# Kernel tuning notes

Measured on AMD Instinct MI355X. Metric: run time of the kernel, lower is better.

The kernel has to match this reference:

```python
import jax, jax.numpy as jnp
import numpy as np

HID = 256   # hidden_dim
P = 16      # pool_size
EPS = 1e-5


def _ln(x, g, b):
    m = x.mean(-1, keepdims=True)
    v = x.var(-1, keepdims=True)
    return (x - m) * jax.lax.rsqrt(v + EPS) * g + b


def setup_inputs() -> dict:
    key = jax.random.key(0)
    ks = jax.random.split(key, 12)
    B, Cf, H, W = 8, 512, 64, 64
    Cg = Cf // 2
    Co = Cf // 2
    s = 0.02
    d = {}
    d['e_f'] = jax.random.normal(ks[0], (B, Cf, H, W), jnp.float32)
    d['e_g'] = jax.random.normal(ks[1], (B, Cg, H, W), jnp.float32)
    d['l_feat'] = jax.random.normal(ks[2], (B, 768, 20), jnp.float32)
    d['l_mask'] = jnp.ones((B, 20, 1), jnp.float32)
    d['ln_f_g'] = jnp.ones((Cf,), jnp.float32)
    d['ln_f_b'] = jnp.zeros((Cf,), jnp.float32)
    d['ln_g_g'] = jnp.ones((Cg,), jnp.float32)
    d['ln_g_b'] = jnp.zeros((Cg,), jnp.float32)
    d['wq'] = jax.random.normal(ks[3], (Cf, HID), jnp.float32) * s
    d['bq'] = jnp.zeros((HID,), jnp.float32)
    d['wk'] = jax.random.normal(ks[4], (Cg, HID), jnp.float32) * s
    d['bk'] = jnp.zeros((HID,), jnp.float32)
    d['wv'] = jax.random.normal(ks[5], (Cg, HID), jnp.float32) * s
    d['bv'] = jnp.zeros((HID,), jnp.float32)
    d['wo'] = jax.random.normal(ks[6], (HID, HID), jnp.float32) * s
    d['bo'] = jnp.zeros((HID,), jnp.float32)
    d['dw_k'] = jax.random.normal(ks[7], (HID, 1, 3, 3), jnp.float32) * s  # depthwise kernel (OIHW, I=1)
    d['efp_w'] = jax.random.normal(ks[8], (HID, Cf), jnp.float32) * s     # 1x1 conv v_channels->hidden
    d['efp_b'] = jnp.zeros((HID,), jnp.float32)
    d['outc_w'] = jax.random.normal(ks[9], (Co, HID), jnp.float32) * s    # 1x1 conv hidden->out
    d['outc_b'] = jnp.zeros((Co,), jnp.float32)
    d['bn_g'] = jnp.ones((Co,), jnp.float32)
    d['bn_b'] = jnp.zeros((Co,), jnp.float32)
    d['bn_m'] = jnp.zeros((Co,), jnp.float32)
    d['bn_v'] = jnp.ones((Co,), jnp.float32)
    return d


def reference(e_f, e_g, l_feat, l_mask, ln_f_g, ln_f_b, ln_g_g, ln_g_b,
              wq, bq, wk, bk, wv, bv, wo, bo, dw_k, efp_w, efp_b,
              outc_w, outc_b, bn_g, bn_b, bn_m, bn_v):
    B, Cf, H, W = e_f.shape
    # Q = w_qi(LN(e_f))                                  (B, HW, HID)
    q = _ln(e_f.transpose(0, 2, 3, 1), ln_f_g, ln_f_b).reshape(B, H * W, Cf) @ wq + bq
    # K/V projections from LN(e_g)
    g = _ln(e_g.transpose(0, 2, 3, 1), ln_g_g, ln_g_b).reshape(B, H * W, -1)
    k = (g @ wk + bk).reshape(B, H, W, HID)
    v = (g @ wv + bv).reshape(B, H, W, HID)
    # 16x16 max/avg pooling -> (B, Hp*Wp, HID)
    k = jnp.max(k.reshape(B, H // P, P, W // P, P, HID), axis=(2, 4)).reshape(B, -1, HID)
    v = jnp.mean(v.reshape(B, H // P, P, W // P, P, HID), axis=(2, 4)).reshape(B, -1, HID)
    # pooled attention
    attn = jax.nn.softmax(jnp.einsum('bqd,bkd->bqk', q, k) * (HID ** -0.5), axis=-1)
    a_i = jnp.einsum('bqk,bkd->bqd', attn, v)  # (B, HW, HID)
    # depthwise 3x3 conv on Q (NCHW)
    q_nchw = q.reshape(B, H, W, HID).transpose(0, 3, 1, 2)
    dw = jax.lax.conv_general_dilated(q_nchw, dw_k, (1, 1), [(1, 1), (1, 1)],
                                      feature_group_count=HID)
    combined = dw + a_i.reshape(B, H, W, HID).transpose(0, 3, 1, 2)
    comb = combined.transpose(0, 2, 3, 1).reshape(B, H * W, HID) @ wo + bo
    comb = comb.reshape(B, H, W, HID).transpose(0, 3, 1, 2)
    # 1x1 proj of e_f, elementwise gate
    efp = jnp.einsum('bchw,oc->bohw', e_f, efp_w) + efp_b[None, :, None, None]
    e_a = efp * comb
    # out: 1x1 conv + BN (inference) + ReLU (dropout inactive in eval)
    out = jnp.einsum('bchw,oc->bohw', e_a, outc_w) + outc_b[None, :, None, None]
    scale = (bn_g * jax.lax.rsqrt(bn_v + EPS))[None, :, None, None]
    out = (out - bn_m[None, :, None, None]) * scale + bn_b[None, :, None, None]
    return jax.nn.relu(out)
```

## Files before the change

kernel.cpp:

```cpp
#include <hip/hip_runtime.h>
#include <math.h>

#define EPS 1e-5f

typedef __attribute__((ext_vector_type(8))) short bf16x8;
typedef __attribute__((ext_vector_type(4))) float f32x4;

__device__ __forceinline__ unsigned short f2bf(float f) {
    unsigned int u = __float_as_uint(f);
    u += 0x7fff + ((u >> 16) & 1);
    return (unsigned short)(u >> 16);
}
__device__ __forceinline__ float bf2f(unsigned short h) {
    return __uint_as_float(((unsigned int)h) << 16);
}
__device__ __forceinline__ float lof(unsigned int u) {
    return __uint_as_float(u << 16);
}
__device__ __forceinline__ float hif(unsigned int u) {
    return __uint_as_float(u & 0xffff0000u);
}
__device__ __forceinline__ void async16(void* lds, const void* g) {
    __builtin_amdgcn_global_load_lds(
        (const __attribute__((address_space(1))) unsigned int*)g,
        (__attribute__((address_space(3))) unsigned int*)lds, 16, 0, 0);
}

__global__ __launch_bounds__(256) void prep_all(
    const float* __restrict__ lnfg, const float* __restrict__ lnfb,
    const float* __restrict__ wq, const float* __restrict__ bq,
    const float* __restrict__ efpw, const float* __restrict__ efpb,
    const float* __restrict__ lngg, const float* __restrict__ lngb,
    const float* __restrict__ wk, const float* __restrict__ bk,
    const float* __restrict__ wv, const float* __restrict__ bv,
    const float* __restrict__ wo, const float* __restrict__ outcw,
    const float* __restrict__ outcb, const float* __restrict__ bng,
    const float* __restrict__ bnb, const float* __restrict__ bnm,
    const float* __restrict__ bnv, const float* __restrict__ dwk,
    unsigned short* __restrict__ Wb1t, unsigned short* __restrict__ Wb2t,
    unsigned short* __restrict__ Wot, unsigned short* __restrict__ Woc,
    float* __restrict__ dwt,
    float* __restrict__ cs1, float* __restrict__ cst1,
    float* __restrict__ cs2, float* __restrict__ cst2,
    float* __restrict__ scv, float* __restrict__ shv)
{
    int idx = blockIdx.x * 256 + threadIdx.x;
    if (idx < 262144) {
        int n = idx >> 9, k = idx & 511;
        float v = (n < 256) ? lnfg[k] * wq[k * 256 + n]
                            : efpw[(size_t)(n - 256) * 512 + k];
        Wb1t[idx] = f2bf(v);
    } else if (idx < 327680) {
        int j = idx - 262144; int n = j >> 8, k = j & 255;
        Wb2t[j] = f2bf(lngg[k] * wk[k * 256 + n]);
    } else if (idx < 393216) {
        int j = idx - 327680; int n = j >> 8, k = j & 255;
        Wot[j] = f2bf(wo[k * 256 + n]);
    } else if (idx < 458752) {
        int j = idx - 393216;
        Woc[j] = f2bf(outcw[j]);
    } else if (idx < 461056) {
        int j = idx - 458752; int tap = j >> 8, ch = j & 255;
        dwt[j] = dwk[ch * 9 + tap];
    } else if (idx < 462336) {
        int j = idx - 461056;
        if (j < 256) {
            int n = j; float cs = 0.f, ct = 0.f;
            for (int k = 0; k < 512; k++) {
                float w = wq[k * 256 + n];
                cs += lnfg[k] * w; ct += lnfb[k] * w;
            }
            cs1[n] = cs; cst1[n] = ct + bq[n];
        } else if (j < 512) {
            cs1[j] = 0.f; cst1[j] = efpb[j - 256];
        } else if (j < 768) {
            int n = j - 512; float cs = 0.f, ct = 0.f;
            for (int k = 0; k < 256; k++) {
                float w = wk[k * 256 + n];
                cs += lngg[k] * w; ct += lngb[k] * w;
            }
            cs2[n] = cs; cst2[n] = ct + bk[n];
        } else if (j < 1024) {
            int n = j - 768; float cs = 0.f, ct = 0.f;
            for (int k = 0; k < 256; k++) {
                float w = wv[k * 256 + n];
                cs += lngg[k] * w; ct += lngb[k] * w;
            }
            cs2[256 + n] = cs; cst2[256 + n] = ct + bv[n];
        } else {
            int n = j - 1024;
            float s = bng[n] * rsqrtf(bnv[n] + EPS);
            scv[n] = s;
            shv[n] = (outcb[n] - bnm[n]) * s + bnb[n];
        }
    }
}

__global__ __launch_bounds__(256) void transpose_fg(
    const float* __restrict__ ef, const float* __restrict__ eg,
    unsigned short* __restrict__ ef_bf, unsigned short* __restrict__ eg_bf,
    float* __restrict__ pf, float* __restrict__ pfq,
    float* __restrict__ pg, float* __restrict__ pgq)
{
    __shared__ float tile[16384];
    int id = blockIdx.x;
    const float* src; unsigned short* dst; float* ps; float* pq;
    int C, cblk, b, p0;
    if (id < 1024) {
        src = ef; dst = ef_bf; ps = pf; pq = pfq; C = 512;
        b = id >> 7; cblk = (id >> 4) & 7; p0 = (id & 15) * 256;
    } else {
        id -= 1024;
        src = eg; dst = eg_bf; ps = pg; pq = pgq; C = 256;
        b = id >> 6; cblk = (id >> 4) & 3; p0 = (id & 15) * 256;
    }
    int c0 = cblk * 64;
    const float* s = src + ((size_t)b * C + c0) * 4096 + p0;
    int t = threadIdx.x;
    int wave = t >> 6, lane = t & 63;

    float4 rr[16];
#pragma unroll
    for (int i = 0; i < 16; i++) {
        int c = wave * 16 + i;
        rr[i] = *(const float4*)(s + (size_t)c * 4096 + lane * 4);
    }
#pragma unroll
    for (int i = 0; i < 16; i++) {
        int c = wave * 16 + i;
        int rq = (c + (c >> 3)) & 63;
        *(float4*)&tile[c * 256 + (((lane + rq) & 63) << 2)] = rr[i];
    }
    __syncthreads();

    {
        int pq4 = t >> 2, pr4 = t & 3;
        float sm = 0.f, sq = 0.f;
#pragma unroll
        for (int c = 0; c < 64; c++) {
            int rq = (c + (c >> 3)) & 63;
            float v = tile[c * 256 + (((pq4 + rq) & 63) << 2) + pr4];
            sm += v; sq += v * v;
        }
        ps[cblk * 32768 + b * 4096 + p0 + t] = sm;
        pq[cblk * 32768 + b * 4096 + p0 + t] = sq;
    }

    unsigned short* d = dst + ((size_t)(b * 4096 + p0)) * C + c0;
    int pr = t >> 3, c8 = (t & 7) * 8;
#pragma unroll
    for (int i = 0; i < 8; i++) {
        int p = i * 32 + pr;
        int pq4 = p >> 2, pr4 = p & 3;
        float v[8];
#pragma unroll
        for (int j = 0; j < 8; j++) {
            int c = c8 + j;
            int rq = (c + (c >> 3)) & 63;
            v[j] = tile[c * 256 + (((pq4 + rq) & 63) << 2) + pr4];
        }
        uint4 pk;
        pk.x = (unsigned)f2bf(v[0]) | ((unsigned)f2bf(v[1]) << 16);
        pk.y = (unsigned)f2bf(v[2]) | ((unsigned)f2bf(v[3]) << 16);
        pk.z = (unsigned)f2bf(v[4]) | ((unsigned)f2bf(v[5]) << 16);
        pk.w = (unsigned)f2bf(v[6]) | ((unsigned)f2bf(v[7]) << 16);
        *(uint4*)(d + (size_t)p * C + c8) = pk;
    }
}

template<int K>
__device__ __forceinline__ void mfma_core(
    const unsigned short* __restrict__ A, const unsigned short* __restrict__ Bt,
    int m0, int n0, unsigned short* As, unsigned short* Bs, f32x4 acc[4][4])
{
    const int tid = threadIdx.x;
    const int wave = tid >> 6, lane = tid & 63;
    const int wm = (wave & 1) * 64, wn = (wave >> 1) * 64;
#pragma unroll
    for (int i = 0; i < 4; i++)
#pragma unroll
        for (int j = 0; j < 4; j++) acc[i][j] = (f32x4){0.f, 0.f, 0.f, 0.f};

    const int srow = wave * 32 + (lane >> 3);
    const int sg = (lane & 7) ^ ((lane >> 3) & 7);
    const unsigned short* ga = A + (size_t)(m0 + srow) * K + sg * 8;
    const unsigned short* gb = Bt + (size_t)(n0 + srow) * K + sg * 8;

    for (int k0 = 0; k0 < K; k0 += 64) {
#pragma unroll
        for (int t = 0; t < 4; t++) {
            async16(As + (wave * 32 + t * 8) * 64, ga + (size_t)t * 8 * K + k0);
            async16(Bs + (wave * 32 + t * 8) * 64, gb + (size_t)t * 8 * K + k0);
        }
        __syncthreads();
#pragma unroll
        for (int ks = 0; ks < 2; ks++) {
            bf16x8 af[4], bfr[4];
            int kb = ks * 4 + (lane >> 4);
            int slot = (kb ^ (lane & 7)) * 8;
#pragma unroll
            for (int i = 0; i < 4; i++) {
                int m = wm + i * 16 + (lane & 15);
                af[i] = *(const bf16x8*)&As[m * 64 + slot];
                int n = wn + i * 16 + (lane & 15);
                bfr[i] = *(const bf16x8*)&Bs[n * 64 + slot];
            }
#pragma unroll
            for (int i = 0; i < 4; i++)
#pragma unroll
                for (int j = 0; j < 4; j++)
                    acc[i][j] = __builtin_amdgcn_mfma_f32_16x16x32_bf16(
                        af[i], bfr[j], acc[i][j], 0, 0, 0);
        }
        __syncthreads();
    }
}

__global__ __launch_bounds__(256, 2) void gemm1_mfma(
    const unsigned short* __restrict__ ef_bf, const unsigned short* __restrict__ Wb1t,
    const float* __restrict__ cs1, const float* __restrict__ cst1,
    const float* __restrict__ pf, const float* __restrict__ pfq,
    unsigned short* __restrict__ qbuf, unsigned short* __restrict__ efpbuf)
{
    __shared__ unsigned short As[128 * 64];
    __shared__ unsigned short Bs[256 * 64];
    __shared__ float smf[128], srf[128];
    f32x4 acc[4][8];
    const int tid = threadIdx.x;
    const int wave = tid >> 6, lane = tid & 63;
    const int wm = (wave & 1) * 64, wn = (wave >> 1) * 128;
    const int m0 = blockIdx.x * 128, n0 = blockIdx.y * 256;

    if (tid < 128) {
        int gm = m0 + tid;
        float s = 0.f, q = 0.f;
#pragma unroll
        for (int i = 0; i < 8; i++) { s += pf[i * 32768 + gm]; q += pfq[i * 32768 + gm]; }
        float m = s * (1.f / 512.f);
        smf[tid] = m;
        srf[tid] = rsqrtf(q * (1.f / 512.f) - m * m + EPS);
    }

#pragma unroll
    for (int i = 0; i < 4; i++)
#pragma unroll
        for (int j = 0; j < 8; j++) acc[i][j] = (f32x4){0.f, 0.f, 0.f, 0.f};

    const int srow = lane >> 3;
    const int sg = (lane & 7) ^ (srow & 7);
    const unsigned short* ga = ef_bf + (size_t)(m0 + wave * 32 + srow) * 512 + sg * 8;
    const unsigned short* gb = Wb1t + (size_t)(n0 + wave * 64 + srow) * 512 + sg * 8;

    for (int k0 = 0; k0 < 512; k0 += 64) {
#pragma unroll
        for (int t = 0; t < 4; t++)
            async16(As + (wave * 32 + t * 8) * 64, ga + (size_t)t * 8 * 512 + k0);
#pragma unroll
        for (int t = 0; t < 8; t++)
            async16(Bs + (wave * 64 + t * 8) * 64, gb + (size_t)t * 8 * 512 + k0);
        __syncthreads();
#pragma unroll
        for (int ks = 0; ks < 2; ks++) {
            bf16x8 af[4], bfr[8];
            int kb = ks * 4 + (lane >> 4);
            int slot = (kb ^ (lane & 7)) * 8;
#pragma unroll
            for (int i = 0; i < 4; i++)
                af[i] = *(const bf16x8*)&As[(wm + i * 16 + (lane & 15)) * 64 + slot];
#pragma unroll
            for (int j = 0; j < 8; j++)
                bfr[j] = *(const bf16x8*)&Bs[(wn + j * 16 + (lane & 15)) * 64 + slot];
#pragma unroll
            for (int i = 0; i < 4; i++)
#pragma unroll
                for (int j = 0; j < 8; j++)
                    acc[i][j] = __builtin_amdgcn_mfma_f32_16x16x32_bf16(
                        af[i], bfr[j], acc[i][j], 0, 0, 0);
        }
        __syncthreads();
    }

    bool isq = (n0 == 0);
#pragma unroll
    for (int i = 0; i < 4; i++) {
#pragma unroll
        for (int r = 0; r < 4; r++) {
            int lm = wm + i * 16 + ((lane >> 4) * 4) + r;
            int gm = m0 + lm;
            float mean = smf[lm], rs = srf[lm];
#pragma unroll
            for (int j = 0; j < 8; j++) {
                int nn = wn + j * 16 + (lane & 15);
                float v = acc[i][j][r];
                if (isq) {
                    int n = nn;
                    float o = rs * (v - mean * cs1[n]) + cst1[n];
                    qbuf[(size_t)gm * 256 + nn] = f2bf(o);
                } else {
                    int n = nn + 256;
                    efpbuf[(size_t)gm * 256 + nn] = f2bf(v + cst1[n]);
                }
            }
        }
    }
}

__global__ __launch_bounds__(256) void gemm2k_mfma(
    const unsigned short* __restrict__ eg_bf, const unsigned short* __restrict__ Wb2t,
    const float* __restrict__ cs2, const float* __restrict__ cst2,
    const float* __restrict__ pg, const float* __restrict__ pgq,
    float* __restrict__ mg, float* __restrict__ rg,
    unsigned short* __restrict__ kfull)
{
    __shared__ unsigned short As[8192], Bs[8192];
    __shared__ float smg[128], srg[128];
    f32x4 acc[4][4];
    int m0 = blockIdx.x * 128, n0 = blockIdx.y * 128;
    int tid = threadIdx.x;

    if (tid < 128) {
        int gm = m0 + tid;
        float s = 0.f, q = 0.f;
#pragma unroll
        for (int i = 0; i < 4; i++) { s += pg[i * 32768 + gm]; q += pgq[i * 32768 + gm]; }
        float m = s * (1.f / 256.f);
        float r = rsqrtf(q * (1.f / 256.f) - m * m + EPS);
        smg[tid] = m; srg[tid] = r;
        if (n0 == 0) { mg[gm] = m; rg[gm] = r; }
    }

    mfma_core<256>(eg_bf, Wb2t, m0, n0, As, Bs, acc);
    int lane = tid & 63, wave = tid >> 6;
    int wm = (wave & 1) * 64, wn = (wave >> 1) * 64;
#pragma unroll
    for (int i = 0; i < 4; i++) {
#pragma unroll
        for (int r = 0; r < 4; r++) {
            int lm = wm + i * 16 + ((lane >> 4) * 4) + r;
            int gm = m0 + lm;
            float mean = smg[lm], rs = srg[lm];
#pragma unroll
            for (int j = 0; j < 4; j++) {
                int n = n0 + wn + j * 16 + (lane & 15);
                float o = rs * (acc[i][j][r] - mean * cs2[n]) + cst2[n];
                kfull[(size_t)gm * 256 + n] = f2bf(o);
            }
        }
    }
}

__global__ __launch_bounds__(256) void gemm34_mfma(
    const unsigned short* __restrict__ comb, const unsigned short* __restrict__ Wot,
    const float* __restrict__ bo, const unsigned short* __restrict__ efp,
    const unsigned short* __restrict__ Woc,
    const float* __restrict__ scv, const float* __restrict__ shv,
    float* __restrict__ outp)
{
    __shared__ unsigned short As[64 * 64];
    __shared__ unsigned short Bs[256 * 64];
    __shared__ unsigned short eat[64 * 256];
    const int tid = threadIdx.x;
    const int wave = tid >> 6, lane = tid & 63;
    const int m0 = blockIdx.x * 64;

    const int srow = lane >> 3;
    const int sg = (lane & 7) ^ (srow & 7);

    f32x4 acc[4][4];
#pragma unroll
    for (int i = 0; i < 4; i++)
#pragma unroll
        for (int j = 0; j < 4; j++) acc[i][j] = (f32x4){0.f, 0.f, 0.f, 0.f};

    const unsigned short* ga = comb + (size_t)(m0 + wave * 16 + srow) * 256 + sg * 8;
    const unsigned short* gb = Wot + (size_t)(wave * 64 + srow) * 256 + sg * 8;

    for (int k0 = 0; k0 < 256; k0 += 64) {
#pragma unroll
        for (int t = 0; t < 2; t++)
            async16(As + (wave * 16 + t * 8) * 64, ga + (size_t)t * 8 * 256 + k0);
#pragma unroll
        for (int t = 0; t < 8; t++)
            async16(Bs + (wave * 64 + t * 8) * 64, gb + (size_t)t * 8 * 256 + k0);
        __syncthreads();
#pragma unroll
        for (int ks = 0; ks < 2; ks++) {
            bf16x8 af[4], bfr[4];
            int kb = ks * 4 + (lane >> 4);
            int slot = (kb ^ (lane & 7)) * 8;
#pragma unroll
            for (int i = 0; i < 4; i++) {
                af[i]  = *(const bf16x8*)&As[(i * 16 + (lane & 15)) * 64 + slot];
                bfr[i] = *(const bf16x8*)&Bs[(wave * 64 + i * 16 + (lane & 15)) * 64 + slot];
            }
#pragma unroll
            for (int i = 0; i < 4; i++)
#pragma unroll
                for (int j = 0; j < 4; j++)
                    acc[i][j] = __builtin_amdgcn_mfma_f32_16x16x32_bf16(
                        af[i], bfr[j], acc[i][j], 0, 0, 0);
        }
        __syncthreads();
    }

    float bo4[4];
#pragma unroll
    for (int j = 0; j < 4; j++) bo4[j] = bo[wave * 64 + j * 16 + (lane & 15)];
#pragma unroll
    for (int i = 0; i < 4; i++) {
#pragma unroll
        for (int r = 0; r < 4; r++) {
            int pos = i * 16 + ((lane >> 4) * 4) + r;
#pragma unroll
            for (int j = 0; j < 4; j++) {
                int n = wave * 64 + j * 16 + (lane & 15);
                float o = (acc[i][j][r] + bo4[j])
                          * bf2f(efp[(size_t)(m0 + pos) * 256 + n]);
                int o8 = j * 2 + ((lane >> 3) & 1);
                int slot = o8 ^ (pos & 7);
                eat[pos * 256 + wave * 64 + slot * 8 + (lane & 7)] = f2bf(o);
            }
        }
    }

    f32x4 acc2[4][4];
#pragma unroll
    for (int i = 0; i < 4; i++)
#pragma unroll
        for (int j = 0; j < 4; j++) acc2[i][j] = (f32x4){0.f, 0.f, 0.f, 0.f};

    const unsigned short* gw = Woc + (size_t)(wave * 64 + srow) * 256 + sg * 8;
    for (int k0 = 0; k0 < 256; k0 += 64) {
#pragma unroll
        for (int t = 0; t < 8; t++)
            async16(Bs + (wave * 64 + t * 8) * 64, gw + (size_t)t * 8 * 256 + k0);
        __syncthreads();
        int kc = k0 >> 6;
#pragma unroll
        for (int ks = 0; ks < 2; ks++) {
            bf16x8 af2[4], bf2_[4];
            int kb = ks * 4 + (lane >> 4);
            int slot = (kb ^ (lane & 7)) * 8;
#pragma unroll
            for (int i = 0; i < 4; i++) {
                af2[i]  = *(const bf16x8*)&Bs[(wave * 64 + i * 16 + (lane & 15)) * 64 + slot];
                bf2_[i] = *(const bf16x8*)&eat[(i * 16 + (lane & 15)) * 256 + kc * 64 + slot];
            }
#pragma unroll
            for (int i = 0; i < 4; i++)
#pragma unroll
                for (int j = 0; j < 4; j++)
                    acc2[i][j] = __builtin_amdgcn_mfma_f32_16x16x32_bf16(
                        af2[i], bf2_[j], acc2[i][j], 0, 0, 0);
        }
        __syncthreads();
    }

#pragma unroll
    for (int i = 0; i < 4; i++) {
#pragma unroll
        for (int r = 0; r < 4; r++) {
            int co = wave * 64 + i * 16 + ((lane >> 4) * 4) + r;
            float s = scv[co], hh = shv[co];
#pragma unroll
            for (int j = 0; j < 4; j++) {
                int p = m0 + j * 16 + (lane & 15);
                float o = fmaxf(fmaf(acc2[i][j][r], s, hh), 0.f);
                outp[((size_t)(p >> 12)) * 1048576 + (size_t)co * 4096 + (p & 4095)] = o;
            }
        }
    }
}

__global__ __launch_bounds__(256) void pool_phase(
    const unsigned short* __restrict__ kfull, const float* __restrict__ eg,
    const float* __restrict__ rg, const float* __restrict__ mg,
    unsigned short* __restrict__ kpb, float* __restrict__ s1,
    float* __restrict__ s0)
{
    __shared__ float smem[4352];
    int id = blockIdx.x;
    int t = threadIdx.x;
    if (id < 128) {
        int b = id >> 4, cell = id & 15;
        int hp = cell >> 2, wp = cell & 3;
        int g8 = t & 31, rr = t >> 5;
        float kmx[8];
#pragma unroll
        for (int j = 0; j < 8; j++) kmx[j] = -3.402823466e38f;
#pragma unroll
        for (int rsub = 0; rsub < 2; rsub++) {
            int r = rr * 2 + rsub;
            int prow = (hp * 16 + r) * 64 + wp * 16;
            for (int cl = 0; cl < 16; cl++) {
                size_t basei = ((size_t)(b * 4096 + prow + cl)) * 256 + g8 * 8;
                uint4 kv = *(const uint4*)(kfull + basei);
                kmx[0] = fmaxf(kmx[0], lof(kv.x)); kmx[1] = fmaxf(kmx[1], hif(kv.x));
                kmx[2] = fmaxf(kmx[2], lof(kv.y)); kmx[3] = fmaxf(kmx[3], hif(kv.y));
                kmx[4] = fmaxf(kmx[4], lof(kv.z)); kmx[5] = fmaxf(kmx[5], hif(kv.z));
                kmx[6] = fmaxf(kmx[6], lof(kv.w)); kmx[7] = fmaxf(kmx[7], hif(kv.w));
            }
        }
#pragma unroll
        for (int j = 0; j < 8; j++) smem[rr * 256 + g8 * 8 + j] = kmx[j];
        __syncthreads();
        float m = smem[t];
#pragma unroll
        for (int r2 = 1; r2 < 8; r2++) m = fmaxf(m, smem[r2 * 256 + t]);
        kpb[(size_t)(b * 16 + cell) * 256 + t] = f2bf(m);
    } else {
        int id2 = id - 128;
        int b = id2 >> 6, hp = (id2 >> 4) & 3, cgrp = id2 & 15;
        int rr = t >> 4, cq = t & 15, cx = cq >> 2;
        int p = (hp * 16 + rr) * 64 + cq * 4;
        float4 w4 = *(const float4*)&rg[b * 4096 + p];
        float part[16];
        const float* egb = eg + ((size_t)b * 256 + cgrp * 16) * 4096 + p;
#pragma unroll
        for (int cc = 0; cc < 16; cc++) {
            float4 v4 = *(const float4*)(egb + (size_t)cc * 4096);
            part[cc] = w4.x * v4.x + w4.y * v4.y + w4.z * v4.z + w4.w * v4.w;
        }
#pragma unroll
        for (int cc = 0; cc < 16; cc++) smem[t * 16 + cc] = part[cc];
        if (cgrp == 0) {
            float4 m4 = *(const float4*)&mg[b * 4096 + p];
            smem[4096 + t] = w4.x * m4.x + w4.y * m4.y + w4.z * m4.z + w4.w * m4.w;
        }
        __syncthreads();
        if (t < 64) {
            int cx2 = t >> 4, cc = t & 15;
            float sacc = 0.f;
#pragma unroll
            for (int rr2 = 0; rr2 < 16; rr2++)
#pragma unroll
                for (int dq = 0; dq < 4; dq++)
                    sacc += smem[(rr2 * 16 + cx2 * 4 + dq) * 16 + cc];
            s1[((size_t)(b * 16 + hp * 4 + cx2)) * 256 + cgrp * 16 + cc] = sacc;
        }
        if (cgrp == 0 && t < 4) {
            float sacc = 0.f;
#pragma unroll
            for (int rr2 = 0; rr2 < 16; rr2++)
#pragma unroll
                for (int dq = 0; dq < 4; dq++)
                    sacc += smem[4096 + rr2 * 16 + t * 4 + dq];
            s0[b * 16 + hp * 4 + t] = sacc;
        }
    }
}

__global__ __launch_bounds__(256) void vpool_gemm(
    const float* __restrict__ s1, const float* __restrict__ s0,
    const float* __restrict__ lngg, const float* __restrict__ wv,
    const float* __restrict__ cs2, const float* __restrict__ cst2,
    float* __restrict__ vp)
{
    int cell = blockIdx.x;
    int n = threadIdx.x;
    const float* s1r = s1 + (size_t)cell * 256;
    float acc = 0.f;
    for (int c = 0; c < 256; c++)
        acc = fmaf(lngg[c] * s1r[c], wv[c * 256 + n], acc);
    vp[(size_t)cell * 256 + n] = acc * (1.f / 256.f)
        - (s0[cell] * (1.f / 256.f)) * cs2[256 + n] + cst2[256 + n];
}

__global__ __launch_bounds__(256) void combined_dw(
    const unsigned short* __restrict__ qbuf, const unsigned short* __restrict__ kpb,
    const float* __restrict__ vp, const float* __restrict__ dwt,
    unsigned short* __restrict__ combined)
{
    __shared__ float attns[256];
    int wave = threadIdx.x >> 6, lane = threadIdx.x & 63;
    int id = blockIdx.x;
    int b = id & 7, seg = id >> 3;
    int pidx0 = seg * 16;

    if (wave == 0) {
        int fr = lane & 15, quad = lane >> 4;
        const unsigned short* qrow = qbuf + (size_t)(b * 4096 + pidx0 + fr) * 256 + quad * 8;
        const unsigned short* krow = kpb + (size_t)(b * 16 + fr) * 256 + quad * 8;
        f32x4 sacc = {0.f, 0.f, 0.f, 0.f};
#pragma unroll
        for (int ks = 0; ks < 8; ks++) {
            bf16x8 af = *(const bf16x8*)(qrow + ks * 32);
            bf16x8 bf_ = *(const bf16x8*)(krow + ks * 32);
            sacc = __builtin_amdgcn_mfma_f32_16x16x32_bf16(af, bf_, sacc, 0, 0, 0);
        }
#pragma unroll
        for (int r = 0; r < 4; r++) {
            float s = sacc[r] * 0.0625f;
            float mx = s;
#pragma unroll
            for (int off = 8; off >= 1; off >>= 1) mx = fmaxf(mx, __shfl_xor(mx, off));
            float e = __expf(s - mx);
            float sum = e;
#pragma unroll
            for (int off = 8; off >= 1; off >>= 1) sum += __shfl_xor(sum, off);
            attns[(quad * 4 + r) * 16 + fr] = e / sum;
        }
    }
    __syncthreads();

    int pidx = pidx0 + wave * 4;
    int h = pidx >> 6, w0 = pidx & 63;
    int o4 = lane * 4;

    float4 kreg[9];
#pragma unroll
    for (int tap = 0; tap < 9; tap++)
        kreg[tap] = *(const float4*)&dwt[tap * 256 + o4];

    float4 acc[4];
#pragma unroll
    for (int i = 0; i < 4; i++) acc[i] = (float4){0.f, 0.f, 0.f, 0.f};

    const float* arow = attns + (wave * 4) * 16;
#pragma unroll
    for (int c = 0; c < 16; c++) {
        float4 v = *(const float4*)&vp[(size_t)(b * 16 + c) * 256 + o4];
#pragma unroll
        for (int i = 0; i < 4; i++) {
            float a = arow[i * 16 + c];
            acc[i].x = fmaf(a, v.x, acc[i].x); acc[i].y = fmaf(a, v.y, acc[i].y);
            acc[i].z = fmaf(a, v.z, acc[i].z); acc[i].w = fmaf(a, v.w, acc[i].w);
        }
    }
#pragma unroll
    for (int dy = 0; dy < 3; dy++) {
        int hh = h + dy - 1;
        if (hh < 0 || hh > 63) continue;
        const unsigned short* qr = qbuf + ((size_t)(b * 4096 + hh * 64)) * 256;
        float4 ft[6];
#pragma unroll
        for (int c = 0; c < 6; c++) {
            int xx = w0 - 1 + c;
            if (xx < 0 || xx > 63) {
                ft[c] = (float4){0.f, 0.f, 0.f, 0.f};
            } else {
                uint2 qa = *(const uint2*)(qr + (size_t)xx * 256 + o4);
                ft[c] = (float4){lof(qa.x), hif(qa.x), lof(qa.y), hif(qa.y)};
            }
        }
#pragma unroll
        for (int dx = 0; dx < 3; dx++) {
            float4 kk = kreg[dy * 3 + dx];
#pragma unroll
            for (int i = 0; i < 4; i++) {
                float4 qv = ft[i + dx];
                acc[i].x = fmaf(qv.x, kk.x, acc[i].x);
                acc[i].y = fmaf(qv.y, kk.y, acc[i].y);
                acc[i].z = fmaf(qv.z, kk.z, acc[i].z);
                acc[i].w = fmaf(qv.w, kk.w, acc[i].w);
            }
        }
    }
#pragma unroll
    for (int i = 0; i < 4; i++) {
        uint2 pk;
        pk.x = (unsigned)f2bf(acc[i].x) | ((unsigned)f2bf(acc[i].y) << 16);
        pk.y = (unsigned)f2bf(acc[i].z) | ((unsigned)f2bf(acc[i].w) << 16);
        *(uint2*)(combined + ((size_t)(b * 4096 + pidx + i)) * 256 + o4) = pk;
    }
}

extern "C" void kernel_launch(void* const* d_in, const int* in_sizes, int n_in,
                              void* d_out, int out_size, void* d_ws, size_t ws_size,
                              hipStream_t stream)
{
    const float* e_f   = (const float*)d_in[0];
    const float* e_g   = (const float*)d_in[1];
    const float* lnfg  = (const float*)d_in[4];
    const float* lnfb  = (const float*)d_in[5];
    const float* lngg  = (const float*)d_in[6];
    const float* lngb  = (const float*)d_in[7];
    const float* wq    = (const float*)d_in[8];
    const float* bq    = (const float*)d_in[9];
    const float* wk    = (const float*)d_in[10];
    const float* bk    = (const float*)d_in[11];
    const float* wv    = (const float*)d_in[12];
    const float* bv    = (const float*)d_in[13];
    const float* wo    = (const float*)d_in[14];
    const float* bo    = (const float*)d_in[15];
    const float* dwk   = (const float*)d_in[16];
    const float* efpw  = (const float*)d_in[17];
    const float* efpb  = (const float*)d_in[18];
    const float* outcw = (const float*)d_in[19];
    const float* outcb = (const float*)d_in[20];
    const float* bng   = (const float*)d_in[21];
    const float* bnb   = (const float*)d_in[22];
    const float* bnm   = (const float*)d_in[23];
    const float* bnv   = (const float*)d_in[24];
    float* outp = (float*)d_out;

    char* base = (char*)d_ws;
    auto alloc = [&](size_t bytes) -> char* {
        char* r = base; base += (bytes + 255) & ~(size_t)255; return r;
    };
    float* pf    = (float*)alloc(8 * 32768 * 4);
    float* pfq   = (float*)alloc(8 * 32768 * 4);
    float* pg    = (float*)alloc(4 * 32768 * 4);
    float* pgq   = (float*)alloc(4 * 32768 * 4);
    float* mg    = (float*)alloc(32768 * 4);
    float* rg    = (float*)alloc(32768 * 4);
    float* cs1   = (float*)alloc(512 * 4);
    float* cst1  = (float*)alloc(512 * 4);
    float* cs2   = (float*)alloc(512 * 4);
    float* cst2  = (float*)alloc(512 * 4);
    float* scv   = (float*)alloc(256 * 4);
    float* shv   = (float*)alloc(256 * 4);
    float* dwt   = (float*)alloc(9 * 256 * 4);
    unsigned short* Wb1t = (unsigned short*)alloc(262144 * 2);
    unsigned short* Wb2t = (unsigned short*)alloc(65536 * 2);
    unsigned short* Wot  = (unsigned short*)alloc(65536 * 2);
    unsigned short* Woc  = (unsigned short*)alloc(65536 * 2);
    unsigned short* ef_bf = (unsigned short*)alloc((size_t)32768 * 512 * 2);
    unsigned short* eg_bf = (unsigned short*)alloc((size_t)32768 * 256 * 2);
    unsigned short* qbuf  = (unsigned short*)alloc((size_t)32768 * 256 * 2);
    unsigned short* efpbuf = (unsigned short*)alloc((size_t)32768 * 256 * 2);
    unsigned short* kfull = (unsigned short*)alloc((size_t)32768 * 256 * 2);
    unsigned short* kpb  = (unsigned short*)alloc(128 * 256 * 2);
    float* vp    = (float*)alloc(128 * 256 * 4);
    float* s1    = (float*)alloc(128 * 256 * 4);
    float* s0    = (float*)alloc(128 * 4);

    prep_all<<<1806, 256, 0, stream>>>(
        lnfg, lnfb, wq, bq, efpw, efpb, lngg, lngb, wk, bk, wv, bv, wo,
        outcw, outcb, bng, bnb, bnm, bnv, dwk,
        Wb1t, Wb2t, Wot, Woc, dwt, cs1, cst1, cs2, cst2, scv, shv);
    transpose_fg<<<1536, 256, 0, stream>>>(e_f, e_g, ef_bf, eg_bf,
                                           pf, pfq, pg, pgq);
    gemm1_mfma<<<dim3(256, 2), 256, 0, stream>>>(ef_bf, Wb1t, cs1, cst1, pf, pfq,
                                                 qbuf, efpbuf);
    gemm2k_mfma<<<dim3(256, 2), 256, 0, stream>>>(eg_bf, Wb2t, cs2, cst2, pg, pgq,
                                                  mg, rg, kfull);
    pool_phase<<<640, 256, 0, stream>>>(kfull, e_g, rg, mg, kpb, s1, s0);
    vpool_gemm<<<128, 256, 0, stream>>>(s1, s0, lngg, wv, cs2, cst2, vp);
    combined_dw<<<2048, 256, 0, stream>>>(qbuf, kpb, vp, dwt, kfull);
    gemm34_mfma<<<512, 256, 0, stream>>>(kfull, Wot, bo, efpbuf,
                                         Woc, scv, shv, outp);
}
```

Measured before the change: 320.5 us.

## Fuse NCHW transpose, bf16 cast and LayerNorm stats into projection GEMMs

Removes the separate transpose_fg kernel and its bf16 intermediate buffers. The GEMM kernels now load fp32 NCHW tiles straight into LDS, compute per-pixel LayerNorm sums on the fly, convert to bf16 with a swizzled layout in LDS, and then run MFMA. This saves the global write and re-read of the transposed activations and the partial-stat buffers. In exchange, gemm1 reruns its whole A-tile load and conversion for both output halves (Q and efp), the M tile shrinks to 64, and there are more barriers per k-step with no double buffering.

```diff
diff --git a/kernel.cpp b/kernel.cpp
--- a/kernel.cpp
+++ b/kernel.cpp
@@ -96,103 +96,196 @@
     }
 }
 
-__global__ __launch_bounds__(256) void transpose_fg(
-    const float* __restrict__ ef, const float* __restrict__ eg,
-    unsigned short* __restrict__ ef_bf, unsigned short* __restrict__ eg_bf,
-    float* __restrict__ pf, float* __restrict__ pfq,
-    float* __restrict__ pg, float* __restrict__ pgq)
+__global__ __launch_bounds__(256) void gemm1_direct(
+    const float* __restrict__ ef, const unsigned short* __restrict__ Wb1t,
+    const float* __restrict__ cs1, const float* __restrict__ cst1,
+    unsigned short* __restrict__ qbuf, unsigned short* __restrict__ efpbuf)
 {
-    __shared__ float tile[16384];
-    int id = blockIdx.x;
-    const float* src; unsigned short* dst; float* ps; float* pq;
-    int C, cblk, b, p0;
-    if (id < 1024) {
-        src = ef; dst = ef_bf; ps = pf; pq = pfq; C = 512;
-        b = id >> 7; cblk = (id >> 4) & 7; p0 = (id & 15) * 256;
-    } else {
-        id -= 1024;
-        src = eg; dst = eg_bf; ps = pg; pq = pgq; C = 256;
-        b = id >> 6; cblk = (id >> 4) & 3; p0 = (id & 15) * 256;
-    }
-    int c0 = cblk * 64;
-    const float* s = src + ((size_t)b * C + c0) * 4096 + p0;
-    int t = threadIdx.x;
-    int wave = t >> 6, lane = t & 63;
-
-    float4 rr[16];
-#pragma unroll
-    for (int i = 0; i < 16; i++) {
-        int c = wave * 16 + i;
-        rr[i] = *(const float4*)(s + (size_t)c * 4096 + lane * 4);
-    }
-#pragma unroll
-    for (int i = 0; i < 16; i++) {
-        int c = wave * 16 + i;
-        int rq = (c + (c >> 3)) & 63;
-        *(float4*)&tile[c * 256 + (((lane + rq) & 63) << 2)] = rr[i];
-    }
-    __syncthreads();
-
-    {
-        int pq4 = t >> 2, pr4 = t & 3;
-        float sm = 0.f, sq = 0.f;
-#pragma unroll
-        for (int c = 0; c < 64; c++) {
-            int rq = (c + (c >> 3)) & 63;
-            float v = tile[c * 256 + (((pq4 + rq) & 63) << 2) + pr4];
-            sm += v; sq += v * v;
-        }
-        ps[cblk * 32768 + b * 4096 + p0 + t] = sm;
-        pq[cblk * 32768 + b * 4096 + p0 + t] = sq;
-    }
-
-    unsigned short* d = dst + ((size_t)(b * 4096 + p0)) * C + c0;
-    int pr = t >> 3, c8 = (t & 7) * 8;
-#pragma unroll
-    for (int i = 0; i < 8; i++) {
-        int p = i * 32 + pr;
-        int pq4 = p >> 2, pr4 = p & 3;
-        float v[8];
-#pragma unroll
-        for (int j = 0; j < 8; j++) {
-            int c = c8 + j;
-            int rq = (c + (c >> 3)) & 63;
-            v[j] = tile[c * 256 + (((pq4 + rq) & 63) << 2) + pr4];
-        }
-        uint4 pk;
-        pk.x = (unsigned)f2bf(v[0]) | ((unsigned)f2bf(v[1]) << 16);
-        pk.y = (unsigned)f2bf(v[2]) | ((unsigned)f2bf(v[3]) << 16);
-        pk.z = (unsigned)f2bf(v[4]) | ((unsigned)f2bf(v[5]) << 16);
-        pk.w = (unsigned)f2bf(v[6]) | ((unsigned)f2bf(v[7]) << 16);
-        *(uint4*)(d + (size_t)p * C + c8) = pk;
-    }
-}
-
-template<int K>
-__device__ __forceinline__ void mfma_core(
-    const unsigned short* __restrict__ A, const unsigned short* __restrict__ Bt,
-    int m0, int n0, unsigned short* As, unsigned short* Bs, f32x4 acc[4][4])
-{
+    __shared__ float Asf[64 * 64];
+    __shared__ unsigned short Asb[64 * 64];
+    __shared__ unsigned short Bs[256 * 64];
+    __shared__ float smf[64], srf[64];
     const int tid = threadIdx.x;
     const int wave = tid >> 6, lane = tid & 63;
-    const int wm = (wave & 1) * 64, wn = (wave >> 1) * 64;
+    const int m0 = blockIdx.x * 64;
+    const int b = m0 >> 12, p0 = m0 & 4095;
+
+    const int srow = lane >> 3;
+    const int sg = (lane & 7) ^ (srow & 7);
+    const int oct = tid & 7, mb = tid >> 3;
+
+    float sm0 = 0.f, sq0 = 0.f, sm1 = 0.f, sq1 = 0.f;
+
+    for (int half = 0; half < 2; half++) {
+        f32x4 acc[4][4];
+#pragma unroll
+        for (int i = 0; i < 4; i++)
+#pragma unroll
+            for (int j = 0; j < 4; j++) acc[i][j] = (f32x4){0.f, 0.f, 0.f, 0.f};
+
+        const unsigned short* gb =
+            Wb1t + (size_t)(half * 256 + wave * 64 + srow) * 512 + sg * 8;
+
+        for (int k0 = 0; k0 < 512; k0 += 64) {
+#pragma unroll
+            for (int q = 0; q < 4; q++) {
+                int k = wave * 16 + q * 4 + (lane >> 4);
+                int mc = ((lane & 15) - (k >> 3)) & 15;
+                async16((char*)Asf + (wave * 16 + q * 4) * 256,
+                        ef + ((size_t)(b * 512 + k0 + k)) * 4096 + p0 + mc * 4);
+            }
+#pragma unroll
+            for (int t = 0; t < 8; t++)
+                async16(Bs + (wave * 64 + t * 8) * 64, gb + (size_t)t * 8 * 512 + k0);
+            __syncthreads();
+
+#pragma unroll
+            for (int h = 0; h < 2; h++) {
+                int m = mb + h * 32;
+                int rot = (((m >> 2) + oct) & 15) * 4 + (m & 3);
+                float vv[8];
+#pragma unroll
+                for (int j = 0; j < 8; j++)
+                    vv[j] = Asf[(oct * 8 + j) * 64 + rot];
+                if (half == 0) {
+                    float s = 0.f, q2 = 0.f;
+#pragma unroll
+                    for (int j = 0; j < 8; j++) { s += vv[j]; q2 += vv[j] * vv[j]; }
+                    if (h == 0) { sm0 += s; sq0 += q2; }
+                    else        { sm1 += s; sq1 += q2; }
+                }
+                uint4 pk;
+                pk.x = (unsigned)f2bf(vv[0]) | ((unsigned)f2bf(vv[1]) << 16);
+                pk.y = (unsigned)f2bf(vv[2]) | ((unsigned)f2bf(vv[3]) << 16);
+                pk.z = (unsigned)f2bf(vv[4]) | ((unsigned)f2bf(vv[5]) << 16);
+                pk.w = (unsigned)f2bf(vv[6]) | ((unsigned)f2bf(vv[7]) << 16);
+                *(uint4*)&Asb[m * 64 + (oct ^ (m & 7)) * 8] = pk;
+            }
+            __syncthreads();
+
+#pragma unroll
+            for (int ks = 0; ks < 2; ks++) {
+                bf16x8 af[4], bfr[4];
+                int kb = ks * 4 + (lane >> 4);
+                int slot = (kb ^ (lane & 7)) * 8;
+#pragma unroll
+                for (int i = 0; i < 4; i++) {
+                    af[i]  = *(const bf16x8*)&Asb[(i * 16 + (lane & 15)) * 64 + slot];
+                    bfr[i] = *(const bf16x8*)&Bs[(wave * 64 + i * 16 + (lane & 15)) * 64 + slot];
+                }
+#pragma unroll
+                for (int i = 0; i < 4; i++)
+#pragma unroll
+                    for (int j = 0; j < 4; j++)
+                        acc[i][j] = __builtin_amdgcn_mfma_f32_16x16x32_bf16(
+                            af[i], bfr[j], acc[i][j], 0, 0, 0);
+            }
+            __syncthreads();
+        }
+
+        if (half == 0) {
+#pragma unroll
+            for (int off = 1; off < 8; off <<= 1) {
+                sm0 += __shfl_xor(sm0, off); sq0 += __shfl_xor(sq0, off);
+                sm1 += __shfl_xor(sm1, off); sq1 += __shfl_xor(sq1, off);
+            }
+            if ((tid & 7) == 0) {
+                float mean = sm0 * (1.f / 512.f);
+                smf[mb] = mean;
+                srf[mb] = rsqrtf(sq0 * (1.f / 512.f) - mean * mean + EPS);
+                mean = sm1 * (1.f / 512.f);
+                smf[mb + 32] = mean;
+                srf[mb + 32] = rsqrtf(sq1 * (1.f / 512.f) - mean * mean + EPS);
+            }
+            __syncthreads();
+        }
+
+#pragma unroll
+        for (int i = 0; i < 4; i++) {
+#pragma unroll
+            for (int r = 0; r < 4; r++) {
+                int lm = i * 16 + ((lane >> 4) * 4) + r;
+                int gm = m0 + lm;
+#pragma unroll
+                for (int j = 0; j < 4; j++) {
+                    int nn = wave * 64 + j * 16 + (lane & 15);
+                    float v = acc[i][j][r];
+                    if (half == 0) {
+                        float o = srf[lm] * (v - smf[lm] * cs1[nn]) + cst1[nn];
+                        qbuf[(size_t)gm * 256 + nn] = f2bf(o);
+                    } else {
+                        efpbuf[(size_t)gm * 256 + nn] = f2bf(v + cst1[nn + 256]);
+                    }
+                }
+            }
+        }
+    }
+}
+
+__global__ __launch_bounds__(256) void gemm2k_direct(
+    const float* __restrict__ eg, const unsigned short* __restrict__ Wb2t,
+    const float* __restrict__ cs2, const float* __restrict__ cst2,
+    float* __restrict__ mg, float* __restrict__ rg,
+    unsigned short* __restrict__ kfull)
+{
+    __shared__ float Asf[64 * 64];
+    __shared__ unsigned short Asb[64 * 64];
+    __shared__ unsigned short Bs[256 * 64];
+    __shared__ float smg[64], srg[64];
+    const int tid = threadIdx.x;
+    const int wave = tid >> 6, lane = tid & 63;
+    const int m0 = blockIdx.x * 64;
+    const int b = m0 >> 12, p0 = m0 & 4095;
+
+    const int srow = lane >> 3;
+    const int sg = (lane & 7) ^ (srow & 7);
+    const int oct = tid & 7, mb = tid >> 3;
+
+    float sm0 = 0.f, sq0 = 0.f, sm1 = 0.f, sq1 = 0.f;
+
+    f32x4 acc[4][4];
 #pragma unroll
     for (int i = 0; i < 4; i++)
 #pragma unroll
         for (int j = 0; j < 4; j++) acc[i][j] = (f32x4){0.f, 0.f, 0.f, 0.f};
 
-    const int srow = wave * 32 + (lane >> 3);
-    const int sg = (lane & 7) ^ ((lane >> 3) & 7);
-    const unsigned short* ga = A + (size_t)(m0 + srow) * K + sg * 8;
-    const unsigned short* gb = Bt + (size_t)(n0 + srow) * K + sg * 8;
-
-    for (int k0 = 0; k0 < K; k0 += 64) {
-#pragma unroll
-        for (int t = 0; t < 4; t++) {
-            async16(As + (wave * 32 + t * 8) * 64, ga + (size_t)t * 8 * K + k0);
-            async16(Bs + (wave * 32 + t * 8) * 64, gb + (size_t)t * 8 * K + k0);
-        }
-        __syncthreads();
+    const unsigned short* gb = Wb2t + (size_t)(wave * 64 + srow) * 256 + sg * 8;
+
+    for (int k0 = 0; k0 < 256; k0 += 64) {
+#pragma unroll
+        for (int q = 0; q < 4; q++) {
+            int k = wave * 16 + q * 4 + (lane >> 4);
+            int mc = ((lane & 15) - (k >> 3)) & 15;
+            async16((char*)Asf + (wave * 16 + q * 4) * 256,
+                    eg + ((size_t)(b * 256 + k0 + k)) * 4096 + p0 + mc * 4);
+        }
+#pragma unroll
+        for (int t = 0; t < 8; t++)
+            async16(Bs + (wave * 64 + t * 8) * 64, gb + (size_t)t * 8 * 256 + k0);
+        __syncthreads();
+
+#pragma unroll
+        for (int h = 0; h < 2; h++) {
+            int m = mb + h * 32;
+            int rot = (((m >> 2) + oct) & 15) * 4 + (m & 3);
+            float vv[8];
+#pragma unroll
+            for (int j = 0; j < 8; j++)
+                vv[j] = Asf[(oct * 8 + j) * 64 + rot];
+            float s = 0.f, q2 = 0.f;
+#pragma unroll
+            for (int j = 0; j < 8; j++) { s += vv[j]; q2 += vv[j] * vv[j]; }
+            if (h == 0) { sm0 += s; sq0 += q2; }
+            else        { sm1 += s; sq1 += q2; }
+            uint4 pk;
+            pk.x = (unsigned)f2bf(vv[0]) | ((unsigned)f2bf(vv[1]) << 16);
+            pk.y = (unsigned)f2bf(vv[2]) | ((unsigned)f2bf(vv[3]) << 16);
+            pk.z = (unsigned)f2bf(vv[4]) | ((unsigned)f2bf(vv[5]) << 16);
+            pk.w = (unsigned)f2bf(vv[6]) | ((unsigned)f2bf(vv[7]) << 16);
+            *(uint4*)&Asb[m * 64 + (oct ^ (m & 7)) * 8] = pk;
+        }
+        __syncthreads();
+
 #pragma unroll
         for (int ks = 0; ks < 2; ks++) {
             bf16x8 af[4], bfr[4];
@@ -200,10 +293,8 @@
             int slot = (kb ^ (lane & 7)) * 8;
 #pragma unroll
             for (int i = 0; i < 4; i++) {
-                int m = wm + i * 16 + (lane & 15);
-                af[i] = *(const bf16x8*)&As[m * 64 + slot];
-                int n = wn + i * 16 + (lane & 15);
-                bfr[i] = *(const bf16x8*)&Bs[n * 64 + slot];
+                af[i]  = *(const bf16x8*)&Asb[(i * 16 + (lane & 15)) * 64 + slot];
+                bfr[i] = *(const bf16x8*)&Bs[(wave * 64 + i * 16 + (lane & 15)) * 64 + slot];
             }
 #pragma unroll
             for (int i = 0; i < 4; i++)
@@ -214,136 +305,36 @@
         }
         __syncthreads();
     }
-}
-
-__global__ __launch_bounds__(256, 2) void gemm1_mfma(
-    const unsigned short* __restrict__ ef_bf, const unsigned short* __restrict__ Wb1t,
-    const float* __restrict__ cs1, const float* __restrict__ cst1,
-    const float* __restrict__ pf, const float* __restrict__ pfq,
-    unsigned short* __restrict__ qbuf, unsigned short* __restrict__ efpbuf)
-{
-    __shared__ unsigned short As[128 * 64];
-    __shared__ unsigned short Bs[256 * 64];
-    __shared__ float smf[128], srf[128];
-    f32x4 acc[4][8];
-    const int tid = threadIdx.x;
-    const int wave = tid >> 6, lane = tid & 63;
-    const int wm = (wave & 1) * 64, wn = (wave >> 1) * 128;
-    const int m0 = blockIdx.x * 128, n0 = blockIdx.y * 256;
-
-    if (tid < 128) {
-        int gm = m0 + tid;
-        float s = 0.f, q = 0.f;
-#pragma unroll
-        for (int i = 0; i < 8; i++) { s += pf[i * 32768 + gm]; q += pfq[i * 32768 + gm]; }
-        float m = s * (1.f / 512.f);
-        smf[tid] = m;
-        srf[tid] = rsqrtf(q * (1.f / 512.f) - m * m + EPS);
-    }
-
-#pragma unroll
-    for (int i = 0; i < 4; i++)
-#pragma unroll
-        for (int j = 0; j < 8; j++) acc[i][j] = (f32x4){0.f, 0.f, 0.f, 0.f};
-
-    const int srow = lane >> 3;
-    const int sg = (lane & 7) ^ (srow & 7);
-    const unsigned short* ga = ef_bf + (size_t)(m0 + wave * 32 + srow) * 512 + sg * 8;
-    const unsigned short* gb = Wb1t + (size_t)(n0 + wave * 64 + srow) * 512 + sg * 8;
-
-    for (int k0 = 0; k0 < 512; k0 += 64) {
-#pragma unroll
-        for (int t = 0; t < 4; t++)
-            async16(As + (wave * 32 + t * 8) * 64, ga + (size_t)t * 8 * 512 + k0);
-#pragma unroll
-        for (int t = 0; t < 8; t++)
-            async16(Bs + (wave * 64 + t * 8) * 64, gb + (size_t)t * 8 * 512 + k0);
-        __syncthreads();
-#pragma unroll
-        for (int ks = 0; ks < 2; ks++) {
-            bf16x8 af[4], bfr[8];
-            int kb = ks * 4 + (lane >> 4);
-            int slot = (kb ^ (lane & 7)) * 8;
-#pragma unroll
-            for (int i = 0; i < 4; i++)
-                af[i] = *(const bf16x8*)&As[(wm + i * 16 + (lane & 15)) * 64 + slot];
-#pragma unroll
-            for (int j = 0; j < 8; j++)
-                bfr[j] = *(const bf16x8*)&Bs[(wn + j * 16 + (lane & 15)) * 64 + slot];
-#pragma unroll
-            for (int i = 0; i < 4; i++)
-#pragma unroll
-                for (int j = 0; j < 8; j++)
-                    acc[i][j] = __builtin_amdgcn_mfma_f32_16x16x32_bf16(
-                        af[i], bfr[j], acc[i][j], 0, 0, 0);
-        }
-        __syncthreads();
-    }
-
-    bool isq = (n0 == 0);
+
+#pragma unroll
+    for (int off = 1; off < 8; off <<= 1) {
+        sm0 += __shfl_xor(sm0, off); sq0 += __shfl_xor(sq0, off);
+        sm1 += __shfl_xor(sm1, off); sq1 += __shfl_xor(sq1, off);
+    }
+    if ((tid & 7) == 0) {
+        float mean = sm0 * (1.f / 256.f);
+        float r = rsqrtf(sq0 * (1.f / 256.f) - mean * mean + EPS);
+        smg[mb] = mean; srg[mb] = r;
+        mg[m0 + mb] = mean; rg[m0 + mb] = r;
+        mean = sm1 * (1.f / 256.f);
+        r = rsqrtf(sq1 * (1.f / 256.f) - mean * mean + EPS);
+        smg[mb + 32] = mean; srg[mb + 32] = r;
+        mg[m0 + mb + 32] = mean; rg[m0 + mb + 32] = r;
+    }
+    __syncthreads();
+
 #pragma unroll
     for (int i = 0; i < 4; i++) {
 #pragma unroll
         for (int r = 0; r < 4; r++) {
-            int lm = wm + i * 16 + ((lane >> 4) * 4) + r;
-            int gm = m0 + lm;
-            float mean = smf[lm], rs = srf[lm];
-#pragma unroll
-            for (int j = 0; j < 8; j++) {
-                int nn = wn + j * 16 + (lane & 15);
-                float v = acc[i][j][r];
-                if (isq) {
-                    int n = nn;
-                    float o = rs * (v - mean * cs1[n]) + cst1[n];
-                    qbuf[(size_t)gm * 256 + nn] = f2bf(o);
-                } else {
-                    int n = nn + 256;
-                    efpbuf[(size_t)gm * 256 + nn] = f2bf(v + cst1[n]);
-                }
-            }
-        }
-    }
-}
-
-__global__ __launch_bounds__(256) void gemm2k_mfma(
-    const unsigned short* __restrict__ eg_bf, const unsigned short* __restrict__ Wb2t,
-    const float* __restrict__ cs2, const float* __restrict__ cst2,
-    const float* __restrict__ pg, const float* __restrict__ pgq,
-    float* __restrict__ mg, float* __restrict__ rg,
-    unsigned short* __restrict__ kfull)
-{
-    __shared__ unsigned short As[8192], Bs[8192];
-    __shared__ float smg[128], srg[128];
-    f32x4 acc[4][4];
-    int m0 = blockIdx.x * 128, n0 = blockIdx.y * 128;
-    int tid = threadIdx.x;
-
-    if (tid < 128) {
-        int gm = m0 + tid;
-        float s = 0.f, q = 0.f;
-#pragma unroll
-        for (int i = 0; i < 4; i++) { s += pg[i * 32768 + gm]; q += pgq[i * 32768 + gm]; }
-        float m = s * (1.f / 256.f);
-        float r = rsqrtf(q * (1.f / 256.f) - m * m + EPS);
-        smg[tid] = m; srg[tid] = r;
-        if (n0 == 0) { mg[gm] = m; rg[gm] = r; }
-    }
-
-    mfma_core<256>(eg_bf, Wb2t, m0, n0, As, Bs, acc);
-    int lane = tid & 63, wave = tid >> 6;
-    int wm = (wave & 1) * 64, wn = (wave >> 1) * 64;
-#pragma unroll
-    for (int i = 0; i < 4; i++) {
-#pragma unroll
-        for (int r = 0; r < 4; r++) {
-            int lm = wm + i * 16 + ((lane >> 4) * 4) + r;
+            int lm = i * 16 + ((lane >> 4) * 4) + r;
             int gm = m0 + lm;
             float mean = smg[lm], rs = srg[lm];
 #pragma unroll
             for (int j = 0; j < 4; j++) {
-                int n = n0 + wn + j * 16 + (lane & 15);
-                float o = rs * (acc[i][j][r] - mean * cs2[n]) + cst2[n];
-                kfull[(size_t)gm * 256 + n] = f2bf(o);
+                int nn = wave * 64 + j * 16 + (lane & 15);
+                float o = rs * (acc[i][j][r] - mean * cs2[nn]) + cst2[nn];
+                kfull[(size_t)gm * 256 + nn] = f2bf(o);
             }
         }
     }
@@ -698,10 +689,6 @@
     auto alloc = [&](size_t bytes) -> char* {
         char* r = base; base += (bytes + 255) & ~(size_t)255; return r;
     };
-    float* pf    = (float*)alloc(8 * 32768 * 4);
-    float* pfq   = (float*)alloc(8 * 32768 * 4);
-    float* pg    = (float*)alloc(4 * 32768 * 4);
-    float* pgq   = (float*)alloc(4 * 32768 * 4);
     float* mg    = (float*)alloc(32768 * 4);
     float* rg    = (float*)alloc(32768 * 4);
     float* cs1   = (float*)alloc(512 * 4);
@@ -715,8 +702,6 @@
     unsigned short* Wb2t = (unsigned short*)alloc(65536 * 2);
     unsigned short* Wot  = (unsigned short*)alloc(65536 * 2);
     unsigned short* Woc  = (unsigned short*)alloc(65536 * 2);
-    unsigned short* ef_bf = (unsigned short*)alloc((size_t)32768 * 512 * 2);
-    unsigned short* eg_bf = (unsigned short*)alloc((size_t)32768 * 256 * 2);
     unsigned short* qbuf  = (unsigned short*)alloc((size_t)32768 * 256 * 2);
     unsigned short* efpbuf = (unsigned short*)alloc((size_t)32768 * 256 * 2);
     unsigned short* kfull = (unsigned short*)alloc((size_t)32768 * 256 * 2);
@@ -729,12 +714,8 @@
         lnfg, lnfb, wq, bq, efpw, efpb, lngg, lngb, wk, bk, wv, bv, wo,
         outcw, outcb, bng, bnb, bnm, bnv, dwk,
         Wb1t, Wb2t, Wot, Woc, dwt, cs1, cst1, cs2, cst2, scv, shv);
-    transpose_fg<<<1536, 256, 0, stream>>>(e_f, e_g, ef_bf, eg_bf,
-                                           pf, pfq, pg, pgq);
-    gemm1_mfma<<<dim3(256, 2), 256, 0, stream>>>(ef_bf, Wb1t, cs1, cst1, pf, pfq,
-                                                 qbuf, efpbuf);
-    gemm2k_mfma<<<dim3(256, 2), 256, 0, stream>>>(eg_bf, Wb2t, cs2, cst2, pg, pgq,
-                                                  mg, rg, kfull);
+    gemm1_direct<<<512, 256, 0, stream>>>(e_f, Wb1t, cs1, cst1, qbuf, efpbuf);
+    gemm2k_direct<<<512, 256, 0, stream>>>(e_g, Wb2t, cs2, cst2, mg, rg, kfull);
     pool_phase<<<640, 256, 0, stream>>>(kfull, e_g, rg, mg, kpb, s1, s0);
     vpool_gemm<<<128, 256, 0, stream>>>(s1, s0, lngg, wv, cs2, cst2, vp);
     combined_dw<<<2048, 256, 0, stream>>>(qbuf, kpb, vp, dwt, kfull);
```

After: 348.1 us. 8.6% more time.
